# Kernel tuning notes

Measured on AMD Instinct MI355X. Metric: run time of the kernel, lower is better.

The kernel has to match this reference:

```python
import jax, jax.numpy as jnp
import numpy as np

B, L0, L1, NS, D, H, NL, HM = 16, 512, 256, 32, 256, 8, 4, 4
T = L0 + L1 + NS + 1
HD = D // H
EPS = 1e-5
SCALE = HD ** -0.5


def setup_inputs() -> dict:
    key = jax.random.key(0)
    ks = jax.random.split(key, 20)
    s = 0.02
    return {
        'seq_tokens_0': jax.random.normal(ks[0], (B, L0, D), jnp.float32),
        'seq_tokens_1': jax.random.normal(ks[1], (B, L1, D), jnp.float32),
        'seq_lens_0': jax.random.randint(ks[2], (B,), 0, L0),
        'seq_lens_1': jax.random.randint(ks[3], (B,), 0, L1),
        'ns_tokens': jax.random.normal(ks[4], (B, NS, D), jnp.float32),
        'domain_emb': jax.random.normal(ks[5], (2, D), jnp.float32) * s,
        'cls_token': jax.random.normal(ks[6], (1, 1, D), jnp.float32) * s,
        'ln1_w': jnp.ones((NL, D), jnp.float32),
        'ln1_b': jnp.zeros((NL, D), jnp.float32),
        'qkv_w': jax.random.normal(ks[7], (NL, D, 3 * D), jnp.float32) * s,
        'qkv_b': jnp.zeros((NL, 3 * D), jnp.float32),
        'out_w': jax.random.normal(ks[8], (NL, D, D), jnp.float32) * s,
        'out_b': jnp.zeros((NL, D), jnp.float32),
        'ln2_w': jnp.ones((NL, D), jnp.float32),
        'ln2_b': jnp.zeros((NL, D), jnp.float32),
        'ffn1_w': jax.random.normal(ks[9], (NL, D, HM * D), jnp.float32) * s,
        'ffn1_b': jnp.zeros((NL, HM * D), jnp.float32),
        'ffn2_w': jax.random.normal(ks[10], (NL, HM * D, D), jnp.float32) * s,
        'ffn2_b': jnp.zeros((NL, D), jnp.float32),
        'fln_w': jnp.ones((D,), jnp.float32),
        'fln_b': jnp.zeros((D,), jnp.float32),
    }


def _ln(x, w, b):
    m = jnp.mean(x, -1, keepdims=True)
    v = jnp.var(x, -1, keepdims=True)
    return (x - m) * jax.lax.rsqrt(v + EPS) * w + b


def _build_mask(seq_lens_0, seq_lens_1):
    # static block structure: intra-domain causal, S<->NS bidirectional, CLS sink row
    base = jnp.zeros((T, T), bool)
    base = base.at[:L0, :L0].set(jnp.tril(jnp.ones((L0, L0), bool)))
    base = base.at[L0:L0 + L1, L0:L0 + L1].set(jnp.tril(jnp.ones((L1, L1), bool)))
    ns_s, ns_e = L0 + L1, L0 + L1 + NS
    base = base.at[:ns_s, ns_s:ns_e].set(True)   # S -> NS
    base = base.at[ns_s:ns_e, :ns_e].set(True)   # NS -> S and NS -> NS
    base = base.at[T - 1, :ns_e].set(True)       # CLS reads all S/NS
    base = base.at[T - 1, T - 1].set(True)       # CLS reads itself
    # per-batch padding mask on keys of each seq segment
    kv = jnp.ones((B, T), bool)
    kv = kv.at[:, :L0].set(jnp.arange(L0)[None, :] < seq_lens_0[:, None])
    kv = kv.at[:, L0:L0 + L1].set(jnp.arange(L1)[None, :] < seq_lens_1[:, None])
    return base[None] & kv[:, None, :]  # [B, T, T]


def _attention(x, mask, qkv_w, qkv_b, out_w, out_b):
    qkv = (x @ qkv_w + qkv_b).reshape(B, T, 3, H, HD)
    q, k, v = qkv[:, :, 0], qkv[:, :, 1], qkv[:, :, 2]
    scores = jnp.einsum('bqhd,bkhd->bhqk', q, k) * SCALE
    m = mask[:, None]  # [B,1,T,T]
    s = jnp.where(m, scores, -jnp.inf)
    any_valid = jnp.any(m, -1, keepdims=True)
    mx = jnp.where(any_valid, jnp.max(s, -1, keepdims=True), 0.0)
    e = jnp.exp(s - mx)  # masked entries exp(-inf)=0
    denom = jnp.sum(e, -1, keepdims=True)
    probs = e / jnp.maximum(denom, 1e-30)  # fully-masked rows -> zeros
    out = jnp.einsum('bhqk,bkhd->bqhd', probs, v).reshape(B, T, D)
    return out @ out_w + out_b


def reference(seq_tokens_0, seq_tokens_1, seq_lens_0, seq_lens_1, ns_tokens,
              domain_emb, cls_token, ln1_w, ln1_b, qkv_w, qkv_b, out_w, out_b,
              ln2_w, ln2_b, ffn1_w, ffn1_b, ffn2_w, ffn2_b, fln_w, fln_b):
    t0 = seq_tokens_0 + domain_emb[0][None, None, :]
    t1 = seq_tokens_1 + domain_emb[1][None, None, :]
    cls = jnp.broadcast_to(cls_token, (B, 1, D))
    x = jnp.concatenate([t0, t1, ns_tokens, cls], axis=1)  # [B,T,D]
    mask = _build_mask(seq_lens_0, seq_lens_1)
    for l in range(NL):
        x = x + _attention(_ln(x, ln1_w[l], ln1_b[l]), mask,
                           qkv_w[l], qkv_b[l], out_w[l], out_b[l])
        h = _ln(x, ln2_w[l], ln2_b[l])
        h = jax.nn.gelu(h @ ffn1_w[l] + ffn1_b[l], approximate=False)
        x = x + h @ ffn2_w[l] + ffn2_b[l]
    x = _ln(x, fln_w, fln_b)
    return x[:, -1, :]  # CLS state [B,D]
```

## Files before the change

### kernel.cpp

```cpp
#include <hip/hip_runtime.h>
#include <hip/hip_bf16.h>
#include <math.h>

typedef __attribute__((ext_vector_type(8))) unsigned short ushort8;
typedef __attribute__((ext_vector_type(8))) short short8;
typedef __attribute__((ext_vector_type(4))) float f32x4;
typedef __attribute__((ext_vector_type(4))) unsigned short ushort4v;
typedef __attribute__((ext_vector_type(4))) int i32x4;
typedef unsigned int u32;

namespace {
constexpr int B = 16, L0 = 512, L1 = 256, NS = 32, D = 256, H = 8, NL = 4, HM = 4;
constexpr int T = L0 + L1 + NS + 1;
constexpr int HD = D / H;
constexpr int NTOK = B * T;
constexpr int NS_S = L0 + L1;
constexpr int NS_E = NS_S + NS;
constexpr int TPAD = 832;
constexpr float EPS = 1e-5f;
constexpr float SCL2  = 0.17677669529663687f * 1.4426950408889634f;
}

__device__ __forceinline__ ushort f2bf(float f) {
    union { float f; unsigned u; } v; v.f = f;
    return (ushort)((v.u + 0x7fffu + ((v.u >> 16) & 1u)) >> 16);
}

__device__ __forceinline__ u32 cvtpk(float a, float b) {
    u32 r;
    asm("v_cvt_pk_bf16_f32 %0, %1, %2" : "=v"(r) : "v"(a), "v"(b));
    return r;
}

__device__ __forceinline__ void gload_lds16(const void* g, void* l) {
    __builtin_amdgcn_global_load_lds(
        (const __attribute__((address_space(1))) u32*)g,
        (__attribute__((address_space(3))) u32*)l, 16, 0, 0);
}

__device__ __forceinline__ bool any_valid_rows(
    int m0, int rows, const int* __restrict__ len0, const int* __restrict__ len1)
{
    int m1 = m0 + rows; if (m1 > NTOK) m1 = NTOK;
    const int b0 = m0 / T, b1 = (m1 - 1) / T;
    for (int b = b0; b <= b1; ++b) {
        int t0 = m0 - b * T; if (t0 < 0) t0 = 0;
        int t1 = m1 - b * T; if (t1 > T) t1 = T;
        if (t0 < len0[b]) return true;
        if (t1 > L0 && t0 < L0 + len1[b]) return true;
        if (t1 > NS_S) return true;
    }
    return false;
}

__global__ __launch_bounds__(256) void k_wprep(
    const float* __restrict__ src, ushort* __restrict__ dst, int K, int N)
{
    const size_t off = (size_t)blockIdx.z * K * N;
    src += off; dst += off;
    __shared__ float t[32][33];
    const int kb = blockIdx.x * 32, nb = blockIdx.y * 32;
    const int c = threadIdx.x & 31, r8 = threadIdx.x >> 5;
#pragma unroll
    for (int rr = 0; rr < 32; rr += 8)
        t[r8 + rr][c] = src[(size_t)(kb + r8 + rr) * N + nb + c];
    __syncthreads();
#pragma unroll
    for (int rr = 0; rr < 32; rr += 8)
        dst[(size_t)(nb + r8 + rr) * K + kb + c] = f2bf(t[c][r8 + rr]);
}

__global__ __launch_bounds__(256) void k_build_ln(
    const float* __restrict__ s0, const float* __restrict__ s1,
    const float* __restrict__ ns, const float* __restrict__ dom,
    const float* __restrict__ cls, const float* __restrict__ lnw,
    const float* __restrict__ lnb, float* __restrict__ x, ushort* __restrict__ xn)
{
    const int wid = threadIdx.x >> 6, lane = threadIdx.x & 63;
    const int row = blockIdx.x * 4 + wid;
    if (row >= NTOK) return;
    const int b = row / T, t = row % T;
    const int d0 = lane * 4;
    float4 v;
    if (t < L0) {
        v = *(const float4*)(s0 + ((size_t)b * L0 + t) * D + d0);
        float4 dm = *(const float4*)(dom + d0);
        v.x += dm.x; v.y += dm.y; v.z += dm.z; v.w += dm.w;
    } else if (t < NS_S) {
        v = *(const float4*)(s1 + ((size_t)b * L1 + (t - L0)) * D + d0);
        float4 dm = *(const float4*)(dom + D + d0);
        v.x += dm.x; v.y += dm.y; v.z += dm.z; v.w += dm.w;
    } else if (t < NS_E) {
        v = *(const float4*)(ns + ((size_t)b * NS + (t - NS_S)) * D + d0);
    } else {
        v = *(const float4*)(cls + d0);
    }
    *(float4*)(x + (size_t)row * D + d0) = v;
    float s  = v.x + v.y + v.z + v.w;
    float ss = v.x * v.x + v.y * v.y + v.z * v.z + v.w * v.w;
#pragma unroll
    for (int o = 32; o; o >>= 1) { s += __shfl_xor(s, o); ss += __shfl_xor(ss, o); }
    const float mean = s * (1.f / D);
    const float var  = ss * (1.f / D) - mean * mean;
    const float r = rsqrtf(var + EPS);
    float4 wv = *(const float4*)(lnw + d0);
    float4 bv = *(const float4*)(lnb + d0);
    ushort4v o4;
    o4[0] = f2bf((v.x - mean) * r * wv.x + bv.x);
    o4[1] = f2bf((v.y - mean) * r * wv.y + bv.y);
    o4[2] = f2bf((v.z - mean) * r * wv.z + bv.z);
    o4[3] = f2bf((v.w - mean) * r * wv.w + bv.w);
    *(ushort4v*)(xn + (size_t)row * D + d0) = o4;
}

template<bool GELU, bool RES, bool OBF, bool CLSW>
__global__ __launch_bounds__(256) void k_gemm_mfma(
    const ushort* __restrict__ A, const ushort* __restrict__ Wt,
    const float* __restrict__ bias, void* __restrict__ Cout,
    const float* __restrict__ res, const int* __restrict__ len0,
    const int* __restrict__ len1, int M, int N, int K)
{
    __shared__ ushort As[2][128 * 64];
    __shared__ ushort Bs[2][128 * 64];
    const int tid = threadIdx.x;
    const int lane = tid & 63, w = tid >> 6;
    const int lo = lane & 15, g = lane >> 4;
    const int wr = w >> 1, wc = w & 1;
    const int m0 = CLSW ? (((blockIdx.x * T + (T - 1)) >> 7) << 7) : blockIdx.x * 128;
    const int n0 = blockIdx.y * 128;

    if (!CLSW && !any_valid_rows(m0, 128, len0, len1)) return;

    f32x4 zero = {0.f, 0.f, 0.f, 0.f};
    f32x4 acc[4][4];
#pragma unroll
    for (int mi = 0; mi < 4; ++mi)
#pragma unroll
        for (int ni = 0; ni < 4; ++ni) acc[mi][ni] = zero;

    const ushort* srcA[4];
    const ushort* srcB[4];
    int ldsOff[4];
#pragma unroll
    for (int i = 0; i < 4; ++i) {
        const int idx16 = (w * 4 + i) * 64 + lane;
        const int row = idx16 >> 3;
        const int scb = ((idx16 & 7) * 16) ^ ((row & 7) << 4);
        int arow = m0 + row; if (arow >= M) arow = M - 1;
        srcA[i] = A  + (size_t)arow * K + (scb >> 1);
        srcB[i] = Wt + (size_t)(n0 + row) * K + (scb >> 1);
        ldsOff[i] = (w * 4 + i) * 512;
    }

    const int NT = K >> 6;
#pragma unroll
    for (int i = 0; i < 4; ++i) {
        gload_lds16(srcA[i], &As[0][ldsOff[i]]);
        gload_lds16(srcB[i], &Bs[0][ldsOff[i]]);
    }
    asm volatile("s_waitcnt vmcnt(0)");
    __syncthreads();

    for (int t = 0; t < NT; ++t) {
        const int buf = t & 1;
        if (t + 1 < NT) {
            const int nb = buf ^ 1, ko = (t + 1) * 64;
#pragma unroll
            for (int i = 0; i < 4; ++i) {
                gload_lds16(srcA[i] + ko, &As[nb][ldsOff[i]]);
                gload_lds16(srcB[i] + ko, &Bs[nb][ldsOff[i]]);
            }
        }
#pragma unroll
        for (int kk = 0; kk < 2; ++kk) {
            const int kb = (kk * 64 + g * 16) ^ ((lo & 7) << 4);
            short8 af[4], bfr[4];
#pragma unroll
            for (int mi = 0; mi < 4; ++mi)
                af[mi] = *(const short8*)&As[buf][(wr * 64 + mi * 16 + lo) * 64 + (kb >> 1)];
#pragma unroll
            for (int ni = 0; ni < 4; ++ni)
                bfr[ni] = *(const short8*)&Bs[buf][(wc * 64 + ni * 16 + lo) * 64 + (kb >> 1)];
#pragma unroll
            for (int mi = 0; mi < 4; ++mi)
#pragma unroll
                for (int ni = 0; ni < 4; ++ni)
                    acc[mi][ni] = __builtin_amdgcn_mfma_f32_16x16x32_bf16(
                        af[mi], bfr[ni], acc[mi][ni], 0, 0, 0);
        }
        asm volatile("s_waitcnt vmcnt(0)");
        __syncthreads();
    }

    float bv[4];
#pragma unroll
    for (int ni = 0; ni < 4; ++ni) bv[ni] = bias[n0 + wc * 64 + ni * 16 + lo];
#pragma unroll
    for (int mi = 0; mi < 4; ++mi) {
#pragma unroll
        for (int i = 0; i < 4; ++i) {
            const int row = m0 + wr * 64 + mi * 16 + g * 4 + i;
            if (row >= M) continue;
#pragma unroll
            for (int ni = 0; ni < 4; ++ni) {
                const int col = n0 + wc * 64 + ni * 16 + lo;
                float v = acc[mi][ni][i] + bv[ni];
                if (GELU) v = 0.5f * v * (1.0f + erff(v * 0.70710678118654752f));
                if (RES)  v += res[(size_t)row * N + col];
                if (OBF) ((ushort*)Cout)[(size_t)row * N + col] = f2bf(v);
                else     ((float*)Cout)[(size_t)row * N + col] = v;
            }
        }
    }
}

template<int MODE, bool CLSW>
__global__ __launch_bounds__(256) void k_gemm_fused(
    const ushort* __restrict__ A, const ushort* __restrict__ Wt,
    const float* __restrict__ bias, const float* __restrict__ res,
    const float* __restrict__ lnw, const float* __restrict__ lnb,
    float* __restrict__ xout, ushort* __restrict__ xnout,
    float* __restrict__ dout, const int* __restrict__ len0,
    const int* __restrict__ len1, int M, int K)
{
    __shared__ ushort As[2][64 * 64];
    __shared__ ushort Bs[2][256 * 64];
    __shared__ float redS[64][4];
    __shared__ float redQ[64][4];
    const int tid = threadIdx.x;
    const int lane = tid & 63, w = tid >> 6;
    const int lo = lane & 15, g = lane >> 4;
    const int m0 = CLSW ? (((blockIdx.x * T + (T - 1)) >> 6) << 6) : blockIdx.x * 64;

    if (!CLSW && !any_valid_rows(m0, 64, len0, len1)) return;

    f32x4 zero = {0.f, 0.f, 0.f, 0.f};
    f32x4 acc[4][4];
#pragma unroll
    for (int mi = 0; mi < 4; ++mi)
#pragma unroll
        for (int ni = 0; ni < 4; ++ni) acc[mi][ni] = zero;

    const ushort* srcA[2]; int ldsOffA[2];
    const ushort* srcB[8]; int ldsOffB[8];
#pragma unroll
    for (int j = 0; j < 2; ++j) {
        const int idx16 = j * 256 + tid;
        const int row = idx16 >> 3;
        const int scb = ((idx16 & 7) * 16) ^ ((row & 7) << 4);
        int arow = m0 + row; if (arow >= M) arow = M - 1;
        srcA[j] = A + (size_t)arow * K + (scb >> 1);
        ldsOffA[j] = idx16 * 8;
    }
#pragma unroll
    for (int j = 0; j < 8; ++j) {
        const int idx16 = j * 256 + tid;
        const int row = idx16 >> 3;
        const int scb = ((idx16 & 7) * 16) ^ ((row & 7) << 4);
        srcB[j] = Wt + (size_t)row * K + (scb >> 1);
        ldsOffB[j] = idx16 * 8;
    }

    const int NT = K >> 6;
#pragma unroll
    for (int j = 0; j < 2; ++j) gload_lds16(srcA[j], &As[0][ldsOffA[j]]);
#pragma unroll
    for (int j = 0; j < 8; ++j) gload_lds16(srcB[j], &Bs[0][ldsOffB[j]]);
    asm volatile("s_waitcnt vmcnt(0)");
    __syncthreads();

    for (int t = 0; t < NT; ++t) {
        const int buf = t & 1;
        if (t + 1 < NT) {
            const int nb = buf ^ 1, ko = (t + 1) * 64;
#pragma unroll
            for (int j = 0; j < 2; ++j) gload_lds16(srcA[j] + ko, &As[nb][ldsOffA[j]]);
#pragma unroll
            for (int j = 0; j < 8; ++j) gload_lds16(srcB[j] + ko, &Bs[nb][ldsOffB[j]]);
        }
#pragma unroll
        for (int kk = 0; kk < 2; ++kk) {
            const int kb = (kk * 64 + g * 16) ^ ((lo & 7) << 4);
            short8 af[4], bfr[4];
#pragma unroll
            for (int mi = 0; mi < 4; ++mi)
                af[mi] = *(const short8*)&As[buf][(mi * 16 + lo) * 64 + (kb >> 1)];
#pragma unroll
            for (int ni = 0; ni < 4; ++ni)
                bfr[ni] = *(const short8*)&Bs[buf][(w * 64 + ni * 16 + lo) * 64 + (kb >> 1)];
#pragma unroll
            for (int mi = 0; mi < 4; ++mi)
#pragma unroll
                for (int ni = 0; ni < 4; ++ni)
                    acc[mi][ni] = __builtin_amdgcn_mfma_f32_16x16x32_bf16(
                        af[mi], bfr[ni], acc[mi][ni], 0, 0, 0);
        }
        asm volatile("s_waitcnt vmcnt(0)");
        __syncthreads();
    }

    float bv[4], lw[4], lb[4];
#pragma unroll
    for (int ni = 0; ni < 4; ++ni) {
        const int c = w * 64 + ni * 16 + lo;
        bv[ni] = bias[c]; lw[ni] = lnw[c]; lb[ni] = lnb[c];
    }
#pragma unroll
    for (int mi = 0; mi < 4; ++mi) {
#pragma unroll
        for (int i = 0; i < 4; ++i) {
            const int r64 = mi * 16 + g * 4 + i;
            const int row = m0 + r64;
            float s = 0.f, q = 0.f;
            if (row < M) {
#pragma unroll
                for (int ni = 0; ni < 4; ++ni) {
                    const int col = w * 64 + ni * 16 + lo;
                    float v = acc[mi][ni][i] + bv[ni] + res[(size_t)row * 256 + col];
                    acc[mi][ni][i] = v;
                    s += v; q += v * v;
                }
                s += __shfl_xor(s, 1); q += __shfl_xor(q, 1);
                s += __shfl_xor(s, 2); q += __shfl_xor(q, 2);
                s += __shfl_xor(s, 4); q += __shfl_xor(q, 4);
                s += __shfl_xor(s, 8); q += __shfl_xor(q, 8);
                if (lo == 0) { redS[r64][w] = s; redQ[r64][w] = q; }
            }
        }
    }
    __syncthreads();
#pragma unroll
    for (int mi = 0; mi < 4; ++mi) {
#pragma unroll
        for (int i = 0; i < 4; ++i) {
            const int r64 = mi * 16 + g * 4 + i;
            const int row = m0 + r64;
            if (row >= M) continue;
            const float S = redS[r64][0] + redS[r64][1] + redS[r64][2] + redS[r64][3];
            const float Q = redQ[r64][0] + redQ[r64][1] + redQ[r64][2] + redQ[r64][3];
            const float mean = S * (1.f / 256.f);
            const float var  = Q * (1.f / 256.f) - mean * mean;
            const float rstd = rsqrtf(var + EPS);
            if (MODE == 0) {
#pragma unroll
                for (int ni = 0; ni < 4; ++ni) {
                    const int col = w * 64 + ni * 16 + lo;
                    const float v = acc[mi][ni][i];
                    xout[(size_t)row * 256 + col] = v;
                    xnout[(size_t)row * 256 + col] = f2bf((v - mean) * rstd * lw[ni] + lb[ni]);
                }
            } else {
                const int bq = row / T;
                const int tq = row - bq * T;
                if (tq == T - 1) {
#pragma unroll
                    for (int ni = 0; ni < 4; ++ni) {
                        const int col = w * 64 + ni * 16 + lo;
                        dout[(size_t)bq * 256 + col] =
                            (acc[mi][ni][i] - mean) * rstd * lw[ni] + lb[ni];
                    }
                }
            }
        }
    }
}

__global__ __launch_bounds__(256) void k_repack(
    const ushort* __restrict__ qkv, ushort* __restrict__ Kb, ushort* __restrict__ Vt,
    const int* __restrict__ len0, const int* __restrict__ len1)
{
    const int bh = blockIdx.x, tt = blockIdx.y;
    const int b = bh >> 3, h = bh & 7;
    const int t0 = tt * 64;
    if (tt < 8)       { if (t0 >= len0[b]) return; }
    else if (tt < 12) { if (t0 >= L0 + len1[b]) return; }
    const int tid = threadIdx.x;
    const int r = tid >> 2, c = tid & 3;
    const int t = t0 + r;
    __shared__ ushort vtile[64][40];
    ushort8 k8 = {0,0,0,0,0,0,0,0}, v8 = {0,0,0,0,0,0,0,0};
    if (t < T) {
        const ushort* kp = qkv + ((size_t)(b * T + t) * 3 + 1) * D + h * HD + c * 8;
        k8 = *(const ushort8*)kp;
        v8 = *(const ushort8*)(kp + D);
    }
    *(ushort8*)(Kb + ((size_t)bh * TPAD + t0 + r) * HD + c * 8) = k8;
    *(ushort8*)&vtile[r][c * 8] = v8;
    __syncthreads();
    const int d = tid >> 3, cc = tid & 7;
    ushort8 o;
#pragma unroll
    for (int j = 0; j < 8; ++j) o[j] = vtile[cc * 8 + j][d];
    *(ushort8*)(Vt + ((size_t)bh * HD + d) * TPAD + t0 + cc * 8) = o;
}

__global__ __launch_bounds__(256) void k_flash(
    const ushort* __restrict__ qkv, const ushort* __restrict__ Kb,
    const ushort* __restrict__ Vt, const int* __restrict__ len0,
    const int* __restrict__ len1, ushort* __restrict__ out)
{
    const int bh = blockIdx.x;
    const int qt = 12 - blockIdx.y;
    const int b = bh >> 3, h = bh & 7;
    const int l0b = len0[b], lim01 = L0 + len1[b];

    const int q0t = qt * 64;
    if (qt < 8)       { if (q0t >= l0b) return; }
    else if (qt < 12) { if (q0t >= lim01) return; }

    const int tid = threadIdx.x, lane = tid & 63, w = tid >> 6;
    const int lo = lane & 15, g = lane >> 4;
    const int b4 = g & 1, b5 = g >> 1;
    const int q = q0t + w * 16 + lo;

    int klo = 0, klim;
    if (q < L0)        klim = q;
    else if (q < NS_S) { klo = L0; klim = q; }
    else if (q < NS_E) klim = NS_E - 1;
    else               klim = q;

    int qrow = q; if (qrow > T - 1) qrow = T - 1;
    short8 qf = *(const short8*)(qkv + ((size_t)(b * T + qrow) * 3) * D + h * HD + g * 8);

    const ushort* Kbase = Kb + (size_t)bh * TPAD * HD;
    const ushort* Vbase = Vt + (size_t)bh * HD * TPAD;

    f32x4 acc0 = {0.f, 0.f, 0.f, 0.f}, acc1 = {0.f, 0.f, 0.f, 0.f};
    float mrow = -1e30f, srow = 0.f;

    const int lt0 = (l0b + 63) >> 6;
    const int lt1 = (lim01 - L0 + 63) >> 6;
    int nc0, nc1;
    if (qt < 8)       { nc0 = min(qt + 1, lt0); nc1 = 0; }
    else if (qt < 12) { nc0 = 0; nc1 = min(qt - 7, lt1); }
    else              { nc0 = lt0; nc1 = lt1; }
    const int ntiles = nc0 + nc1 + 1;
    auto ktile = [&](int it) { return (it < nc0) ? it : (it < nc0 + nc1) ? (8 + it - nc0) : 12; };

    short8 kf[4];
    {
        const int k0 = ktile(0) * 64;
#pragma unroll
        for (int n = 0; n < 4; ++n)
            kf[n] = *(const short8*)(Kbase + (size_t)(k0 + n * 16 + lo) * HD + g * 8);
    }

    for (int it = 0; it < ntiles; ++it) {
        const int k0 = ktile(it) * 64;

        const ushort* V0 = Vbase + k0;
        short8 a00 = *(const short8*)(V0 + (size_t)lo * TPAD + g * 8);
        short8 a01 = *(const short8*)(V0 + (size_t)lo * TPAD + 32 + g * 8);
        short8 a10 = *(const short8*)(V0 + (size_t)(16 + lo) * TPAD + g * 8);
        short8 a11 = *(const short8*)(V0 + (size_t)(16 + lo) * TPAD + 32 + g * 8);

        float pv[4][4];
        float tmax = -1e30f;
#pragma unroll
        for (int n = 0; n < 4; ++n) {
            f32x4 z = {0.f, 0.f, 0.f, 0.f};
            f32x4 sn = __builtin_amdgcn_mfma_f32_16x16x32_bf16(kf[n], qf, z, 0, 0, 0);
#pragma unroll
            for (int i = 0; i < 4; ++i) {
                const int k = k0 + n * 16 + g * 4 + i;
                const bool inNS = (k >= NS_S) & (k < NS_E);
                const bool kval = (k < l0b) | ((k >= L0) & (k < lim01)) | (k >= NS_S);
                const bool m = ((k >= klo) & (k <= klim) & kval) | inNS;
                const float sv = m ? sn[i] * SCL2 : -1e30f;
                pv[n][i] = sv;
                tmax = fmaxf(tmax, sv);
            }
        }

        short8 kf2[4];
        if (it + 1 < ntiles) {
            const int k1 = ktile(it + 1) * 64;
#pragma unroll
            for (int n = 0; n < 4; ++n)
                kf2[n] = *(const short8*)(Kbase + (size_t)(k1 + n * 16 + lo) * HD + g * 8);
        }

        tmax = fmaxf(tmax, __shfl_xor(tmax, 16));
        tmax = fmaxf(tmax, __shfl_xor(tmax, 32));
        const float mnew = fmaxf(mrow, tmax);
        const float scl = exp2f(mrow - mnew);
        mrow = mnew;

        u32 C0[4], C1[4];
        float psum = 0.f;
#pragma unroll
        for (int n = 0; n < 4; ++n) {
            float e0 = exp2f(pv[n][0] - mnew);
            float e1 = exp2f(pv[n][1] - mnew);
            float e2 = exp2f(pv[n][2] - mnew);
            float e3 = exp2f(pv[n][3] - mnew);
            psum += (e0 + e1) + (e2 + e3);
            C0[n] = cvtpk(e0, e1);
            C1[n] = cvtpk(e2, e3);
        }
        psum += __shfl_xor(psum, 16);
        psum += __shfl_xor(psum, 32);
        srow = srow * scl + psum;
#pragma unroll
        for (int i = 0; i < 4; ++i) { acc0[i] *= scl; acc1[i] *= scl; }

        u32 pb0u[4], pb1u[4];
#pragma unroll
        for (int n = 0; n < 4; ++n) {
            const u32 F0 = (u32)__shfl_xor((int)C0[n], 16);
            const u32 F1 = (u32)__shfl_xor((int)C1[n], 16);
            const u32 G00 = b4 ? F0 : C0[n];
            const u32 G01 = b4 ? C0[n] : F0;
            const u32 G10 = b4 ? F1 : C1[n];
            const u32 G11 = b4 ? C1[n] : F1;
            const u32 H00 = (u32)__shfl_xor((int)G00, 32);
            const u32 H01 = (u32)__shfl_xor((int)G01, 32);
            const u32 H10 = (u32)__shfl_xor((int)G10, 32);
            const u32 H11 = (u32)__shfl_xor((int)G11, 32);
            const bool keep = (b5 == b4);
            const u32 S00 = keep ? G00 : H00;
            const u32 S01 = keep ? G01 : H01;
            const u32 S10 = keep ? G10 : H10;
            const u32 S11 = keep ? G11 : H11;
            const bool take = (b5 == (n & 1));
            if ((n >> 1) == 0) {
                pb0u[0] = take ? S00 : pb0u[0];
                pb0u[1] = take ? S10 : pb0u[1];
                pb0u[2] = take ? S01 : pb0u[2];
                pb0u[3] = take ? S11 : pb0u[3];
            } else {
                pb1u[0] = take ? S00 : pb1u[0];
                pb1u[1] = take ? S10 : pb1u[1];
                pb1u[2] = take ? S01 : pb1u[2];
                pb1u[3] = take ? S11 : pb1u[3];
            }
        }
        i32x4 t0 = { (int)pb0u[0], (int)pb0u[1], (int)pb0u[2], (int)pb0u[3] };
        i32x4 t1 = { (int)pb1u[0], (int)pb1u[1], (int)pb1u[2], (int)pb1u[3] };
        const short8 pb0 = __builtin_bit_cast(short8, t0);
        const short8 pb1 = __builtin_bit_cast(short8, t1);

        acc0 = __builtin_amdgcn_mfma_f32_16x16x32_bf16(a00, pb0, acc0, 0, 0, 0);
        acc0 = __builtin_amdgcn_mfma_f32_16x16x32_bf16(a01, pb1, acc0, 0, 0, 0);
        acc1 = __builtin_amdgcn_mfma_f32_16x16x32_bf16(a10, pb0, acc1, 0, 0, 0);
        acc1 = __builtin_amdgcn_mfma_f32_16x16x32_bf16(a11, pb1, acc1, 0, 0, 0);

#pragma unroll
        for (int n = 0; n < 4; ++n) kf[n] = kf2[n];
    }

    if (q < T) {
        const float inv = 1.f / fmaxf(srow, 1e-30f);
        ushort* orow = out + (size_t)(b * T + q) * D + h * HD;
        *(u32*)(orow + g * 4)          = cvtpk(acc0[0] * inv, acc0[1] * inv);
        *(u32*)(orow + g * 4 + 2)      = cvtpk(acc0[2] * inv, acc0[3] * inv);
        *(u32*)(orow + 16 + g * 4)     = cvtpk(acc1[0] * inv, acc1[1] * inv);
        *(u32*)(orow + 16 + g * 4 + 2) = cvtpk(acc1[2] * inv, acc1[3] * inv);
    }
}

extern "C" void kernel_launch(void* const* d_in, const int* in_sizes, int n_in,
                              void* d_out, int out_size, void* d_ws, size_t ws_size,
                              hipStream_t stream)
{
    const float* seq0 = (const float*)d_in[0];
    const float* seq1 = (const float*)d_in[1];
    const int*   len0 = (const int*)d_in[2];
    const int*   len1 = (const int*)d_in[3];
    const float* nst  = (const float*)d_in[4];
    const float* dom  = (const float*)d_in[5];
    const float* cls  = (const float*)d_in[6];
    const float* ln1w = (const float*)d_in[7];
    const float* ln1b = (const float*)d_in[8];
    const float* qkvw = (const float*)d_in[9];
    const float* qkvb = (const float*)d_in[10];
    const float* outw = (const float*)d_in[11];
    const float* outb = (const float*)d_in[12];
    const float* ln2w = (const float*)d_in[13];
    const float* ln2b = (const float*)d_in[14];
    const float* f1w  = (const float*)d_in[15];
    const float* f1b  = (const float*)d_in[16];
    const float* f2w  = (const float*)d_in[17];
    const float* f2b  = (const float*)d_in[18];
    const float* flnw = (const float*)d_in[19];
    const float* flnb = (const float*)d_in[20];

    float*  x   = (float*)d_ws;
    ushort* xn  = (ushort*)(x + (size_t)NTOK * D);
    ushort* big = xn + (size_t)NTOK * D;
    ushort* Kb  = big + (size_t)NTOK * HM * D;
    ushort* Vt  = Kb + (size_t)B * H * TPAD * HD;
    ushort* qkvw_t = Vt + (size_t)B * H * TPAD * HD;
    ushort* outw_t = qkvw_t + (size_t)NL * 768 * 256;
    ushort* f1w_t  = outw_t + (size_t)NL * 256 * 256;
    ushort* f2w_t  = f1w_t  + (size_t)NL * 1024 * 256;

    k_wprep<<<dim3(256 / 32, 768 / 32, NL), 256, 0, stream>>>(qkvw, qkvw_t, 256, 768);
    k_wprep<<<dim3(256 / 32, 256 / 32, NL), 256, 0, stream>>>(outw, outw_t, 256, 256);
    k_wprep<<<dim3(256 / 32, 1024 / 32, NL), 256, 0, stream>>>(f1w, f1w_t, 256, 1024);
    k_wprep<<<dim3(1024 / 32, 256 / 32, NL), 256, 0, stream>>>(f2w, f2w_t, 1024, 256);

    k_build_ln<<<(NTOK + 3) / 4, 256, 0, stream>>>(seq0, seq1, nst, dom, cls,
                                                   ln1w, ln1b, x, xn);

    const int gmm = (NTOK + 127) / 128;
    const int gf  = (NTOK + 63) / 64;

    for (int l = 0; l < NL; ++l) {
        const bool last = (l == NL - 1);
        k_gemm_mfma<false, false, true, false><<<dim3(gmm, 6), 256, 0, stream>>>(
            xn, qkvw_t + (size_t)l * 768 * 256, qkvb + (size_t)l * 3 * D, big, nullptr,
            len0, len1, NTOK, 3 * D, D);
        k_repack<<<dim3(B * H, TPAD / 64), 256, 0, stream>>>(big, Kb, Vt, len0, len1);
        k_flash<<<dim3(B * H, last ? 1 : TPAD / 64), 256, 0, stream>>>(
            big, Kb, Vt, len0, len1, xn);
        if (!last)
            k_gemm_fused<0, false><<<gf, 256, 0, stream>>>(
                xn, outw_t + (size_t)l * 256 * 256, outb + (size_t)l * D, x,
                ln2w + l * D, ln2b + l * D, x, xn, nullptr, len0, len1, NTOK, D);
        else
            k_gemm_fused<0, true><<<B, 256, 0, stream>>>(
                xn, outw_t + (size_t)l * 256 * 256, outb + (size_t)l * D, x,
                ln2w + l * D, ln2b + l * D, x, xn, nullptr, len0, len1, NTOK, D);
        if (!last)
            k_gemm_mfma<true, false, true, false><<<dim3(gmm, 8), 256, 0, stream>>>(
                xn, f1w_t + (size_t)l * 1024 * 256, f1b + (size_t)l * HM * D, big,
                nullptr, len0, len1, NTOK, HM * D, D);
        else
            k_gemm_mfma<true, false, true, true><<<dim3(B, 8), 256, 0, stream>>>(
                xn, f1w_t + (size_t)l * 1024 * 256, f1b + (size_t)l * HM * D, big,
                nullptr, len0, len1, NTOK, HM * D, D);
        if (!last)
            k_gemm_fused<0, false><<<gf, 256, 0, stream>>>(
                big, f2w_t + (size_t)l * 256 * 1024, f2b + (size_t)l * D, x,
                ln1w + (l + 1) * D, ln1b + (l + 1) * D, x, xn, nullptr, len0, len1,
                NTOK, HM * D);
        else
            k_gemm_fused<1, true><<<B, 256, 0, stream>>>(
                big, f2w_t + (size_t)l * 256 * 1024, f2b + (size_t)l * D, x,
                flnw, flnb, nullptr, nullptr, (float*)d_out, len0, len1, NTOK, HM * D);
    }
}
```

Baseline: 478.1 us.

## Merge weight prep kernels, skip Q for non-CLS rows, unroll flash by two

The four weight-transpose launches are merged into one kernel that picks its source matrix from the block index. In the last layer the QKV GEMM is split: K and V are computed for all rows, but Q only for the CLS-containing row tile. The flash attention loop now handles two key tiles per step with a conditional rescale, and drops the register prefetch of the next K tile. This cuts launch count and redundant Q work, at the cost of higher register pressure and lost cross-iteration prefetch in the flash kernel.

```diff
diff --git a/kernel.cpp b/kernel.cpp
--- a/kernel.cpp
+++ b/kernel.cpp
@@ -53,13 +53,24 @@
     return false;
 }
 
-__global__ __launch_bounds__(256) void k_wprep(
-    const float* __restrict__ src, ushort* __restrict__ dst, int K, int N)
+__global__ __launch_bounds__(256) void k_wprep_all(
+    const float* __restrict__ qkvw, const float* __restrict__ outw,
+    const float* __restrict__ f1w, const float* __restrict__ f2w,
+    ushort* __restrict__ qkvt, ushort* __restrict__ outt,
+    ushort* __restrict__ f1t, ushort* __restrict__ f2t)
 {
-    const size_t off = (size_t)blockIdx.z * K * N;
-    src += off; dst += off;
+    int id = blockIdx.x;
+    const float* src; ushort* dst; int K, N;
+    if (id < 768)        { src = qkvw; dst = qkvt; K = 256;  N = 768;  }
+    else if (id < 1024)  { id -= 768;  src = outw; dst = outt; K = 256; N = 256; }
+    else if (id < 2048)  { id -= 1024; src = f1w;  dst = f1t;  K = 256; N = 1024; }
+    else                 { id -= 2048; src = f2w;  dst = f2t;  K = 1024; N = 256; }
+    const int ktiles = K >> 5, per = ktiles * (N >> 5);
+    const int layer = id / per, rem = id % per;
+    const int kb = (rem % ktiles) * 32, nb = (rem / ktiles) * 32;
+    src += (size_t)layer * K * N; dst += (size_t)layer * K * N;
+
     __shared__ float t[32][33];
-    const int kb = blockIdx.x * 32, nb = blockIdx.y * 32;
     const int c = threadIdx.x & 31, r8 = threadIdx.x >> 5;
 #pragma unroll
     for (int rr = 0; rr < 32; rr += 8)
@@ -118,7 +129,7 @@
     const ushort* __restrict__ A, const ushort* __restrict__ Wt,
     const float* __restrict__ bias, void* __restrict__ Cout,
     const float* __restrict__ res, const int* __restrict__ len0,
-    const int* __restrict__ len1, int M, int N, int K)
+    const int* __restrict__ len1, int M, int N, int K, int nOff)
 {
     __shared__ ushort As[2][128 * 64];
     __shared__ ushort Bs[2][128 * 64];
@@ -127,7 +138,7 @@
     const int lo = lane & 15, g = lane >> 4;
     const int wr = w >> 1, wc = w & 1;
     const int m0 = CLSW ? (((blockIdx.x * T + (T - 1)) >> 7) << 7) : blockIdx.x * 128;
-    const int n0 = blockIdx.y * 128;
+    const int n0 = (blockIdx.y + nOff) * 128;
 
     if (!CLSW && !any_valid_rows(m0, 128, len0, len1)) return;
 
@@ -437,73 +448,19 @@
     const int ntiles = nc0 + nc1 + 1;
     auto ktile = [&](int it) { return (it < nc0) ? it : (it < nc0 + nc1) ? (8 + it - nc0) : 12; };
 
-    short8 kf[4];
-    {
-        const int k0 = ktile(0) * 64;
-#pragma unroll
-        for (int n = 0; n < 4; ++n)
-            kf[n] = *(const short8*)(Kbase + (size_t)(k0 + n * 16 + lo) * HD + g * 8);
-    }
-
-    for (int it = 0; it < ntiles; ++it) {
-        const int k0 = ktile(it) * 64;
-
-        const ushort* V0 = Vbase + k0;
-        short8 a00 = *(const short8*)(V0 + (size_t)lo * TPAD + g * 8);
-        short8 a01 = *(const short8*)(V0 + (size_t)lo * TPAD + 32 + g * 8);
-        short8 a10 = *(const short8*)(V0 + (size_t)(16 + lo) * TPAD + g * 8);
-        short8 a11 = *(const short8*)(V0 + (size_t)(16 + lo) * TPAD + 32 + g * 8);
-
-        float pv[4][4];
-        float tmax = -1e30f;
-#pragma unroll
-        for (int n = 0; n < 4; ++n) {
-            f32x4 z = {0.f, 0.f, 0.f, 0.f};
-            f32x4 sn = __builtin_amdgcn_mfma_f32_16x16x32_bf16(kf[n], qf, z, 0, 0, 0);
-#pragma unroll
-            for (int i = 0; i < 4; ++i) {
-                const int k = k0 + n * 16 + g * 4 + i;
-                const bool inNS = (k >= NS_S) & (k < NS_E);
-                const bool kval = (k < l0b) | ((k >= L0) & (k < lim01)) | (k >= NS_S);
-                const bool m = ((k >= klo) & (k <= klim) & kval) | inNS;
-                const float sv = m ? sn[i] * SCL2 : -1e30f;
-                pv[n][i] = sv;
-                tmax = fmaxf(tmax, sv);
-            }
-        }
-
-        short8 kf2[4];
-        if (it + 1 < ntiles) {
-            const int k1 = ktile(it + 1) * 64;
-#pragma unroll
-            for (int n = 0; n < 4; ++n)
-                kf2[n] = *(const short8*)(Kbase + (size_t)(k1 + n * 16 + lo) * HD + g * 8);
-        }
-
-        tmax = fmaxf(tmax, __shfl_xor(tmax, 16));
-        tmax = fmaxf(tmax, __shfl_xor(tmax, 32));
-        const float mnew = fmaxf(mrow, tmax);
-        const float scl = exp2f(mrow - mnew);
-        mrow = mnew;
-
-        u32 C0[4], C1[4];
-        float psum = 0.f;
-#pragma unroll
-        for (int n = 0; n < 4; ++n) {
-            float e0 = exp2f(pv[n][0] - mnew);
-            float e1 = exp2f(pv[n][1] - mnew);
-            float e2 = exp2f(pv[n][2] - mnew);
-            float e3 = exp2f(pv[n][3] - mnew);
-            psum += (e0 + e1) + (e2 + e3);
-            C0[n] = cvtpk(e0, e1);
-            C1[n] = cvtpk(e2, e3);
-        }
-        psum += __shfl_xor(psum, 16);
-        psum += __shfl_xor(psum, 32);
-        srow = srow * scl + psum;
-#pragma unroll
-        for (int i = 0; i < 4; ++i) { acc0[i] *= scl; acc1[i] *= scl; }
-
+    auto maskrow = [&](int k0, int n, const f32x4& sn, float pv[4], float& tmax) {
+#pragma unroll
+        for (int i = 0; i < 4; ++i) {
+            const int k = k0 + n * 16 + g * 4 + i;
+            const bool inNS = (k >= NS_S) & (k < NS_E);
+            const bool kval = (k < l0b) | ((k >= L0) & (k < lim01)) | (k >= NS_S);
+            const bool m = ((k >= klo) & (k <= klim) & kval) | inNS;
+            const float sv = m ? sn[i] * SCL2 : -1e30f;
+            pv[i] = sv;
+            tmax = fmaxf(tmax, sv);
+        }
+    };
+    auto xpose = [&](const u32 C0[4], const u32 C1[4], short8& pb0, short8& pb1) {
         u32 pb0u[4], pb1u[4];
 #pragma unroll
         for (int n = 0; n < 4; ++n) {
@@ -537,16 +494,110 @@
         }
         i32x4 t0 = { (int)pb0u[0], (int)pb0u[1], (int)pb0u[2], (int)pb0u[3] };
         i32x4 t1 = { (int)pb1u[0], (int)pb1u[1], (int)pb1u[2], (int)pb1u[3] };
-        const short8 pb0 = __builtin_bit_cast(short8, t0);
-        const short8 pb1 = __builtin_bit_cast(short8, t1);
-
+        pb0 = __builtin_bit_cast(short8, t0);
+        pb1 = __builtin_bit_cast(short8, t1);
+    };
+
+    for (int it = 0; it < ntiles; ) {
+        const bool has2 = (it + 1 < ntiles);
+        const int kA = ktile(it) * 64;
+        const int kB = has2 ? ktile(it + 1) * 64 : kA;
+
+        short8 kfA[4], kfB[4];
+#pragma unroll
+        for (int n = 0; n < 4; ++n)
+            kfA[n] = *(const short8*)(Kbase + (size_t)(kA + n * 16 + lo) * HD + g * 8);
+        if (has2) {
+#pragma unroll
+            for (int n = 0; n < 4; ++n)
+                kfB[n] = *(const short8*)(Kbase + (size_t)(kB + n * 16 + lo) * HD + g * 8);
+        }
+
+        const ushort* VA = Vbase + kA;
+        short8 a00 = *(const short8*)(VA + (size_t)lo * TPAD + g * 8);
+        short8 a01 = *(const short8*)(VA + (size_t)lo * TPAD + 32 + g * 8);
+        short8 a10 = *(const short8*)(VA + (size_t)(16 + lo) * TPAD + g * 8);
+        short8 a11 = *(const short8*)(VA + (size_t)(16 + lo) * TPAD + 32 + g * 8);
+        short8 e00, e01, e10, e11;
+        if (has2) {
+            const ushort* VB = Vbase + kB;
+            e00 = *(const short8*)(VB + (size_t)lo * TPAD + g * 8);
+            e01 = *(const short8*)(VB + (size_t)lo * TPAD + 32 + g * 8);
+            e10 = *(const short8*)(VB + (size_t)(16 + lo) * TPAD + g * 8);
+            e11 = *(const short8*)(VB + (size_t)(16 + lo) * TPAD + 32 + g * 8);
+        }
+
+        float pvA[4][4], pvB[4][4];
+        float tmax = -1e30f;
+#pragma unroll
+        for (int n = 0; n < 4; ++n) {
+            f32x4 z = {0.f, 0.f, 0.f, 0.f};
+            f32x4 sn = __builtin_amdgcn_mfma_f32_16x16x32_bf16(kfA[n], qf, z, 0, 0, 0);
+            maskrow(kA, n, sn, pvA[n], tmax);
+        }
+        if (has2) {
+#pragma unroll
+            for (int n = 0; n < 4; ++n) {
+                f32x4 z = {0.f, 0.f, 0.f, 0.f};
+                f32x4 sn = __builtin_amdgcn_mfma_f32_16x16x32_bf16(kfB[n], qf, z, 0, 0, 0);
+                maskrow(kB, n, sn, pvB[n], tmax);
+            }
+        }
+
+        tmax = fmaxf(tmax, __shfl_xor(tmax, 16));
+        tmax = fmaxf(tmax, __shfl_xor(tmax, 32));
+        const float mnew = fmaxf(mrow, tmax);
+        if (mnew > mrow) {
+            const float scl = exp2f(mrow - mnew);
+            srow *= scl;
+#pragma unroll
+            for (int i = 0; i < 4; ++i) { acc0[i] *= scl; acc1[i] *= scl; }
+            mrow = mnew;
+        }
+
+        u32 CA0[4], CA1[4], CB0[4], CB1[4];
+        float psum = 0.f;
+#pragma unroll
+        for (int n = 0; n < 4; ++n) {
+            float e0 = exp2f(pvA[n][0] - mrow);
+            float e1 = exp2f(pvA[n][1] - mrow);
+            float e2 = exp2f(pvA[n][2] - mrow);
+            float e3 = exp2f(pvA[n][3] - mrow);
+            psum += (e0 + e1) + (e2 + e3);
+            CA0[n] = cvtpk(e0, e1);
+            CA1[n] = cvtpk(e2, e3);
+        }
+        if (has2) {
+#pragma unroll
+            for (int n = 0; n < 4; ++n) {
+                float e0 = exp2f(pvB[n][0] - mrow);
+                float e1 = exp2f(pvB[n][1] - mrow);
+                float e2 = exp2f(pvB[n][2] - mrow);
+                float e3 = exp2f(pvB[n][3] - mrow);
+                psum += (e0 + e1) + (e2 + e3);
+                CB0[n] = cvtpk(e0, e1);
+                CB1[n] = cvtpk(e2, e3);
+            }
+        }
+        psum += __shfl_xor(psum, 16);
+        psum += __shfl_xor(psum, 32);
+        srow += psum;
+
+        short8 pb0, pb1;
+        xpose(CA0, CA1, pb0, pb1);
         acc0 = __builtin_amdgcn_mfma_f32_16x16x32_bf16(a00, pb0, acc0, 0, 0, 0);
         acc0 = __builtin_amdgcn_mfma_f32_16x16x32_bf16(a01, pb1, acc0, 0, 0, 0);
         acc1 = __builtin_amdgcn_mfma_f32_16x16x32_bf16(a10, pb0, acc1, 0, 0, 0);
         acc1 = __builtin_amdgcn_mfma_f32_16x16x32_bf16(a11, pb1, acc1, 0, 0, 0);
-
-#pragma unroll
-        for (int n = 0; n < 4; ++n) kf[n] = kf2[n];
+        if (has2) {
+            xpose(CB0, CB1, pb0, pb1);
+            acc0 = __builtin_amdgcn_mfma_f32_16x16x32_bf16(e00, pb0, acc0, 0, 0, 0);
+            acc0 = __builtin_amdgcn_mfma_f32_16x16x32_bf16(e01, pb1, acc0, 0, 0, 0);
+            acc1 = __builtin_amdgcn_mfma_f32_16x16x32_bf16(e10, pb0, acc1, 0, 0, 0);
+            acc1 = __builtin_amdgcn_mfma_f32_16x16x32_bf16(e11, pb1, acc1, 0, 0, 0);
+        }
+
+        it += has2 ? 2 : 1;
     }
 
     if (q < T) {
@@ -595,10 +646,8 @@
     ushort* f1w_t  = outw_t + (size_t)NL * 256 * 256;
     ushort* f2w_t  = f1w_t  + (size_t)NL * 1024 * 256;
 
-    k_wprep<<<dim3(256 / 32, 768 / 32, NL), 256, 0, stream>>>(qkvw, qkvw_t, 256, 768);
-    k_wprep<<<dim3(256 / 32, 256 / 32, NL), 256, 0, stream>>>(outw, outw_t, 256, 256);
-    k_wprep<<<dim3(256 / 32, 1024 / 32, NL), 256, 0, stream>>>(f1w, f1w_t, 256, 1024);
-    k_wprep<<<dim3(1024 / 32, 256 / 32, NL), 256, 0, stream>>>(f2w, f2w_t, 1024, 256);
+    k_wprep_all<<<3072, 256, 0, stream>>>(qkvw, outw, f1w, f2w,
+                                          qkvw_t, outw_t, f1w_t, f2w_t);
 
     k_build_ln<<<(NTOK + 3) / 4, 256, 0, stream>>>(seq0, seq1, nst, dom, cls,
                                                    ln1w, ln1b, x, xn);
@@ -608,9 +657,18 @@
 
     for (int l = 0; l < NL; ++l) {
         const bool last = (l == NL - 1);
-        k_gemm_mfma<false, false, true, false><<<dim3(gmm, 6), 256, 0, stream>>>(
-            xn, qkvw_t + (size_t)l * 768 * 256, qkvb + (size_t)l * 3 * D, big, nullptr,
-            len0, len1, NTOK, 3 * D, D);
+        if (!last) {
+            k_gemm_mfma<false, false, true, false><<<dim3(gmm, 6), 256, 0, stream>>>(
+                xn, qkvw_t + (size_t)l * 768 * 256, qkvb + (size_t)l * 3 * D, big, nullptr,
+                len0, len1, NTOK, 3 * D, D, 0);
+        } else {
+            k_gemm_mfma<false, false, true, false><<<dim3(gmm, 4), 256, 0, stream>>>(
+                xn, qkvw_t + (size_t)l * 768 * 256, qkvb + (size_t)l * 3 * D, big, nullptr,
+                len0, len1, NTOK, 3 * D, D, 2);
+            k_gemm_mfma<false, false, true, true><<<dim3(B, 2), 256, 0, stream>>>(
+                xn, qkvw_t + (size_t)l * 768 * 256, qkvb + (size_t)l * 3 * D, big, nullptr,
+                len0, len1, NTOK, 3 * D, D, 0);
+        }
         k_repack<<<dim3(B * H, TPAD / 64), 256, 0, stream>>>(big, Kb, Vt, len0, len1);
         k_flash<<<dim3(B * H, last ? 1 : TPAD / 64), 256, 0, stream>>>(
             big, Kb, Vt, len0, len1, xn);
@@ -625,11 +683,11 @@
         if (!last)
             k_gemm_mfma<true, false, true, false><<<dim3(gmm, 8), 256, 0, stream>>>(
                 xn, f1w_t + (size_t)l * 1024 * 256, f1b + (size_t)l * HM * D, big,
-                nullptr, len0, len1, NTOK, HM * D, D);
+                nullptr, len0, len1, NTOK, HM * D, D, 0);
         else
             k_gemm_mfma<true, false, true, true><<<dim3(B, 8), 256, 0, stream>>>(
                 xn, f1w_t + (size_t)l * 1024 * 256, f1b + (size_t)l * HM * D, big,
-                nullptr, len0, len1, NTOK, HM * D, D);
+                nullptr, len0, len1, NTOK, HM * D, D, 0);
         if (!last)
             k_gemm_fused<0, false><<<gf, 256, 0, stream>>>(
                 big, f2w_t + (size_t)l * 256 * 1024, f2b + (size_t)l * D, x,
```

Result: no change. 479.6 us (+0.3%).
